# Optimization experiments

Measured on AMD Instinct MI355X. Metric: run time of the kernel, lower is better.

The kernel has to match this reference:

```python
import jax, jax.numpy as jnp
import numpy as np

NU, NBU, NI, D, L = 50000, 20000, 100000, 64, 2
C_TEMP = 0.25


def setup_inputs() -> dict:
    key = jax.random.key(0)
    ks = jax.random.split(key, 11)
    B, E_ui, E_ub, E_bi = 2048, 1_500_000, 1_000_000, 1_000_000
    return {
        "users": jax.random.randint(ks[0], (B,), 0, NU, dtype=jnp.int32),
        "bundles": jax.random.randint(ks[1], (B, 2), 0, NBU, dtype=jnp.int32),
        "ui_u": jax.random.randint(ks[2], (E_ui,), 0, NU, dtype=jnp.int32),
        "ui_i": jax.random.randint(ks[3], (E_ui,), 0, NI, dtype=jnp.int32),
        "ub_u": jax.random.randint(ks[4], (E_ub,), 0, NU, dtype=jnp.int32),
        "ub_b": jax.random.randint(ks[5], (E_ub,), 0, NBU, dtype=jnp.int32),
        "bi_b": jax.random.randint(ks[6], (E_bi,), 0, NBU, dtype=jnp.int32),
        "bi_i": jax.random.randint(ks[7], (E_bi,), 0, NI, dtype=jnp.int32),
        "users_feature": jax.random.normal(ks[8], (NU, D), jnp.float32) * 0.1,
        "bundles_feature": jax.random.normal(ks[9], (NBU, D), jnp.float32) * 0.1,
        "items_feature": jax.random.normal(ks[10], (NI, D), jnp.float32) * 0.1,
    }


def _sym_norm_vals(rows, cols, n):
    # laplace_transform: D_r^{-1/2} A D_c^{-1/2}; graph is symmetric so row/col degrees coincide
    deg = jax.ops.segment_sum(jnp.ones(rows.shape, jnp.float32), rows, num_segments=n)
    dinv = 1.0 / (jnp.sqrt(deg) + 1e-8)
    return dinv[rows] * dinv[cols]


def _spmm(rows, cols, vals, feat, n):
    return jax.ops.segment_sum(vals[:, None] * feat[cols], rows, num_segments=n)


def _one_propagate(rows, cols, n, A, Bf):
    vals = _sym_norm_vals(rows, cols, n)
    f = jnp.concatenate([A, Bf], axis=0)  # [n, D]
    acc = f
    for i in range(L):
        f = _spmm(rows, cols, vals, f, n) / (i + 2)
        nrm = jnp.maximum(jnp.linalg.norm(f, axis=1, keepdims=True), 1e-12)
        acc = acc + f / nrm  # sum of L2-normalized layer outputs + layer0
    return acc[: A.shape[0]], acc[A.shape[0]:]


def _bundle_agg(bi_b, bi_i, il_items):
    # row-normalized bundle-item aggregation: diag(1/bundle_size) @ BI
    deg = jax.ops.segment_sum(jnp.ones(bi_b.shape, jnp.float32), bi_b, num_segments=NBU)
    w = (1.0 / (deg + 1e-8))[bi_b]
    return jax.ops.segment_sum(w[:, None] * il_items[bi_i], bi_b, num_segments=NBU)


def _c_loss(pos, aug):
    pos = pos[:, 0, :]
    aug = aug[:, 0, :]
    pos = pos / jnp.maximum(jnp.linalg.norm(pos, axis=1, keepdims=True), 1e-12)
    aug = aug / jnp.maximum(jnp.linalg.norm(aug, axis=1, keepdims=True), 1e-12)
    pos_score = jnp.sum(pos * aug, axis=1) / C_TEMP
    ttl = jnp.matmul(pos, aug.T) / C_TEMP  # [B, B]
    return -jnp.mean(pos_score - jax.nn.logsumexp(ttl, axis=1))


def reference(users, bundles, ui_u, ui_i, ub_u, ub_b, bi_b, bi_i,
              users_feature, bundles_feature, items_feature):
    # item-level graph: [[0, UI], [UI^T, 0]], size NU+NI (symmetric directed edge list)
    il_rows = jnp.concatenate([ui_u, ui_i + NU])
    il_cols = jnp.concatenate([ui_i + NU, ui_u])
    IL_users, IL_items = _one_propagate(il_rows, il_cols, NU + NI, users_feature, items_feature)
    IL_bundles = _bundle_agg(bi_b, bi_i, IL_items)

    # bundle-level graph: [[0, UB], [UB^T, 0]], size NU+NBU
    bl_rows = jnp.concatenate([ub_u, ub_b + NU])
    bl_cols = jnp.concatenate([ub_b + NU, ub_u])
    BL_users, BL_bundles = _one_propagate(bl_rows, bl_cols, NU + NBU, users_feature, bundles_feature)

    nb = bundles.shape[1]
    IL_u = jnp.broadcast_to(IL_users[users][:, None, :], (users.shape[0], nb, D))
    BL_u = jnp.broadcast_to(BL_users[users][:, None, :], (users.shape[0], nb, D))
    IL_b = IL_bundles[bundles]  # [B, nb, D]
    BL_b = BL_bundles[bundles]

    pred = jnp.sum(IL_u * IL_b, axis=2) + jnp.sum(BL_u * BL_b, axis=2)  # [B, 2]
    bpr_loss = -jnp.mean(jax.nn.log_sigmoid(pred[:, 0:1] - pred[:, 1:2]))

    c_loss = 0.5 * (_c_loss(IL_u, BL_u) + _c_loss(IL_b, BL_b))
    return jnp.stack([bpr_loss, c_loss])


if __name__ == "__main__":
    out = reference(**setup_inputs())
    print(out)
```

## Files before the change

### kernel.cpp

```cpp
#include <hip/hip_runtime.h>
#include <hip/hip_bf16.h>
#include <math.h>

static constexpr int NUc  = 50000;
static constexpr int NBUc = 20000;
static constexpr int NIc  = 100000;
static constexpr int NILc = 150000;
static constexpr int NBLc = 70000;
static constexpr int GUB0   = 150016;
static constexpr int GBI0   = 220032;
static constexpr int BK_UB0 = 1172;
static constexpr int BK_BI0 = 1719;
static constexpr int NBK    = 1876;
static constexpr int GTOT   = NBK * 128;

__device__ __forceinline__ float wredsum(float v) {
  #pragma unroll
  for (int m = 32; m >= 1; m >>= 1) v += __shfl_xor(v, m, 64);
  return v;
}
__device__ __forceinline__ float bf2f(unsigned short h) {
  return __uint_as_float(((unsigned int)h) << 16);
}
__device__ __forceinline__ unsigned short f2bf(float f) {
  unsigned int u = __float_as_uint(f);
  return (unsigned short)((u + 0x7FFFu + ((u >> 16) & 1u)) >> 16);
}

__global__ void k_bcount_all(const int* __restrict__ ui_u, const int* __restrict__ ui_i,
                             const int* __restrict__ ub_u, const int* __restrict__ ub_b,
                             const int* __restrict__ bi_b,
                             int E_ui, int E_ub, int E_bi, int* __restrict__ bCnt) {
  __shared__ int hist[NBK];
  for (int i = threadIdx.x; i < NBK; i += 256) hist[i] = 0;
  __syncthreads();
  int b = blockIdx.x;
  if (b < 512) {
    int chunk = (E_ui + 511) / 512, c0 = b * chunk, c1 = min(E_ui, c0 + chunk);
    for (int e = c0 + (int)threadIdx.x; e < c1; e += 256) {
      atomicAdd(&hist[ui_u[e] >> 7], 1);
      atomicAdd(&hist[(ui_i[e] + NUc) >> 7], 1);
    }
  } else if (b < 768) {
    int lb = b - 512, chunk = (E_ub + 255) / 256, c0 = lb * chunk, c1 = min(E_ub, c0 + chunk);
    for (int e = c0 + (int)threadIdx.x; e < c1; e += 256) {
      atomicAdd(&hist[(GUB0 + ub_u[e]) >> 7], 1);
      atomicAdd(&hist[(GUB0 + NUc + ub_b[e]) >> 7], 1);
    }
  } else {
    int lb = b - 768, chunk = (E_bi + 255) / 256, c0 = lb * chunk, c1 = min(E_bi, c0 + chunk);
    for (int e = c0 + (int)threadIdx.x; e < c1; e += 256)
      atomicAdd(&hist[(GBI0 + bi_b[e]) >> 7], 1);
  }
  __syncthreads();
  for (int i = threadIdx.x; i < NBK; i += 256)
    if (hist[i]) atomicAdd(&bCnt[i], hist[i]);
}

__global__ void k_scan2048(const int* __restrict__ in, int n,
                           int* __restrict__ outBase, int* __restrict__ outCur) {
  __shared__ int sh[512];
  int t = threadIdx.x, i0 = 4 * t;
  int v0 = (i0 < n) ? in[i0] : 0;
  int v1 = (i0 + 1 < n) ? in[i0 + 1] : 0;
  int v2 = (i0 + 2 < n) ? in[i0 + 2] : 0;
  int v3 = (i0 + 3 < n) ? in[i0 + 3] : 0;
  int ts = v0 + v1 + v2 + v3;
  sh[t] = ts;
  __syncthreads();
  for (int o = 1; o < 512; o <<= 1) {
    int x = (t >= o) ? sh[t - o] : 0;
    __syncthreads();
    sh[t] += x;
    __syncthreads();
  }
  int ex = sh[t] - ts;
  if (i0 < n)     { outBase[i0] = ex;                    outCur[i0] = ex; }
  if (i0 + 1 < n) { outBase[i0 + 1] = ex + v0;           outCur[i0 + 1] = ex + v0; }
  if (i0 + 2 < n) { outBase[i0 + 2] = ex + v0 + v1;      outCur[i0 + 2] = ex + v0 + v1; }
  if (i0 + 3 < n) { outBase[i0 + 3] = ex + v0 + v1 + v2; outCur[i0 + 3] = ex + v0 + v1 + v2; }
  if (t == 511) outBase[n] = sh[511];
}

__global__ void k_bin_all(const int* __restrict__ ui_u, const int* __restrict__ ui_i,
                          const int* __restrict__ ub_u, const int* __restrict__ ub_b,
                          const int* __restrict__ bi_b, const int* __restrict__ bi_i,
                          int E_ui, int E_ub, int E_bi,
                          int* __restrict__ bCur, unsigned int* __restrict__ binned) {
  __shared__ int hist[NBK];
  __shared__ int base[NBK];
  for (int i = threadIdx.x; i < NBK; i += 256) hist[i] = 0;
  __syncthreads();
  int b = blockIdx.x;
  int c0, c1, seg;
  if (b < 512)      { seg = 0; int ch = (E_ui + 511) / 512; c0 = b * ch; c1 = min(E_ui, c0 + ch); }
  else if (b < 768) { seg = 1; int ch = (E_ub + 255) / 256; c0 = (b - 512) * ch; c1 = min(E_ub, c0 + ch); }
  else              { seg = 2; int ch = (E_bi + 255) / 256; c0 = (b - 768) * ch; c1 = min(E_bi, c0 + ch); }
  for (int e = c0 + (int)threadIdx.x; e < c1; e += 256) {
    if (seg == 0) {
      atomicAdd(&hist[ui_u[e] >> 7], 1);
      atomicAdd(&hist[(ui_i[e] + NUc) >> 7], 1);
    } else if (seg == 1) {
      atomicAdd(&hist[(GUB0 + ub_u[e]) >> 7], 1);
      atomicAdd(&hist[(GUB0 + NUc + ub_b[e]) >> 7], 1);
    } else {
      atomicAdd(&hist[(GBI0 + bi_b[e]) >> 7], 1);
    }
  }
  __syncthreads();
  for (int i = threadIdx.x; i < NBK; i += 256) {
    int h = hist[i];
    base[i] = h ? atomicAdd(&bCur[i], h) : 0;
    hist[i] = 0;
  }
  __syncthreads();
  for (int e = c0 + (int)threadIdx.x; e < c1; e += 256) {
    if (seg == 0) {
      int u = ui_u[e], x = ui_i[e] + NUc;
      int b1 = u >> 7;
      binned[base[b1] + atomicAdd(&hist[b1], 1)] = ((unsigned)(u & 127) << 18) | (unsigned)x;
      int b2 = x >> 7;
      binned[base[b2] + atomicAdd(&hist[b2], 1)] = ((unsigned)(x & 127) << 18) | (unsigned)u;
    } else if (seg == 1) {
      int ul = ub_u[e], bl = NUc + ub_b[e];
      int r1 = GUB0 + ul, r2 = GUB0 + bl;
      int b1 = r1 >> 7;
      binned[base[b1] + atomicAdd(&hist[b1], 1)] = ((unsigned)(r1 & 127) << 18) | (unsigned)bl;
      int b2 = r2 >> 7;
      binned[base[b2] + atomicAdd(&hist[b2], 1)] = ((unsigned)(r2 & 127) << 18) | (unsigned)ul;
    } else {
      int r = GBI0 + bi_b[e];
      int b1 = r >> 7;
      binned[base[b1] + atomicAdd(&hist[b1], 1)] = ((unsigned)(r & 127) << 18) | (unsigned)bi_i[e];
    }
  }
}

__global__ void k_rowhist_all(const unsigned int* __restrict__ binned, const int* __restrict__ bBase,
                              int* __restrict__ cnt) {
  __shared__ int hist[128];
  int bk = blockIdx.x, rowbase = bk << 7;
  int s = bBase[bk], e = bBase[bk + 1];
  if (threadIdx.x < 128) hist[threadIdx.x] = 0;
  __syncthreads();
  for (int i = s + (int)threadIdx.x; i < e; i += 256)
    atomicAdd(&hist[binned[i] >> 18], 1);
  __syncthreads();
  if (threadIdx.x < 128) cnt[rowbase + (int)threadIdx.x] = hist[threadIdx.x];
}

__global__ void k_scan_block_pad(const int* __restrict__ in, int n, int* __restrict__ out,
                                 int* __restrict__ bsum) {
  __shared__ int sh[256];
  int t = threadIdx.x;
  long base = (long)blockIdx.x * 1024 + (long)t * 4;
  int v0 = (base     < n) ? ((in[base]     + 15) & ~15) : 0;
  int v1 = (base + 1 < n) ? ((in[base + 1] + 15) & ~15) : 0;
  int v2 = (base + 2 < n) ? ((in[base + 2] + 15) & ~15) : 0;
  int v3 = (base + 3 < n) ? ((in[base + 3] + 15) & ~15) : 0;
  int tsum = v0 + v1 + v2 + v3;
  sh[t] = tsum;
  __syncthreads();
  for (int o = 1; o < 256; o <<= 1) {
    int x = (t >= o) ? sh[t - o] : 0;
    __syncthreads();
    sh[t] += x;
    __syncthreads();
  }
  int excl = sh[t] - tsum;
  if (t == 255) bsum[blockIdx.x] = sh[255];
  if (base     < n) out[base]     = excl;
  if (base + 1 < n) out[base + 1] = excl + v0;
  if (base + 2 < n) out[base + 2] = excl + v0 + v1;
  if (base + 3 < n) out[base + 3] = excl + v0 + v1 + v2;
}

__global__ void k_scan_bsum(int* __restrict__ bsum, int nb) {
  __shared__ int sh[256];
  int t = threadIdx.x;
  int v = (t < nb) ? bsum[t] : 0;
  sh[t] = v;
  __syncthreads();
  for (int o = 1; o < 256; o <<= 1) {
    int x = (t >= o) ? sh[t - o] : 0;
    __syncthreads();
    sh[t] += x;
    __syncthreads();
  }
  if (t < nb) bsum[t] = sh[t] - v;
}

__global__ void k_scan_add(int* __restrict__ out, int n, const int* __restrict__ bsum) {
  long i = (long)blockIdx.x * 256 + threadIdx.x;
  if (i < n) out[i] += bsum[i >> 10];
}

__global__ void k_csrfill_all(const unsigned int* __restrict__ binned, const int* __restrict__ bBase,
                              const int* __restrict__ rp, int* __restrict__ colv) {
  __shared__ int cur[128];
  int bk = blockIdx.x, rowbase = bk << 7;
  int xb, zpad;
  if (bk < BK_UB0)      { xb = 0;    zpad = NILc; }
  else if (bk < BK_BI0) { xb = GUB0; zpad = GUB0 + NBLc; }
  else                  { xb = 0;    zpad = NIc; }
  int s = bBase[bk], e = bBase[bk + 1];
  if (threadIdx.x < 128) cur[threadIdx.x] = rp[rowbase + (int)threadIdx.x];
  __syncthreads();
  for (int i = s + (int)threadIdx.x; i < e; i += 256) {
    unsigned int pk = binned[i];
    int pos = atomicAdd(&cur[pk >> 18], 1);
    colv[pos] = xb + (int)(pk & 0x3FFFFu);
  }
  __syncthreads();
  if (threadIdx.x < 128) {
    int r = rowbase + (int)threadIdx.x;
    int end = rp[r + 1];
    for (int k = cur[threadIdx.x]; k < end; k++) colv[k] = zpad;
  }
}

__global__ void k_prescale_all(const int* __restrict__ cnt, const float* __restrict__ userF,
                               const float* __restrict__ bundF, const float* __restrict__ itemF,
                               unsigned short* __restrict__ X) {
  long idx = (long)blockIdx.x * 256 + threadIdx.x;
  if (idx >= (long)GBI0 * 64) return;
  int g = (int)(idx >> 6), d = (int)(idx & 63);
  float v = 0.0f;
  if (g < NILc) v = (g < NUc) ? userF[(long)g * 64 + d] : itemF[(long)(g - NUc) * 64 + d];
  else if (g >= GUB0 && g < GUB0 + NBLc) {
    int l = g - GUB0;
    v = (l < NUc) ? userF[(long)l * 64 + d] : bundF[(long)(l - NUc) * 64 + d];
  }
  float dinv = 1.0f / (sqrtf((float)cnt[g]) + 1e-8f);
  X[idx] = f2bf(v * dinv);
}

__global__ void k_spmm_g(const int* __restrict__ rp, const int* __restrict__ cnt,
                         const int* __restrict__ col, const unsigned short* __restrict__ X,
                         unsigned short* __restrict__ outB, float* __restrict__ outInv,
                         float scale, int mulDinv, int n) {
  int row = blockIdx.x * 4 + (threadIdx.x >> 6);
  if (row >= n) return;
  int lane = threadIdx.x & 63, q = lane >> 4, p = lane & 15;
  int s = rp[row], e = rp[row + 1];
  const uint2* Xp = (const uint2*)X + p;
  float a0 = 0.f, a1 = 0.f, a2 = 0.f, a3 = 0.f;
  for (int eo = s + q; eo < e; eo += 16) {
    int c0 = col[eo], c1 = col[eo + 4], c2 = col[eo + 8], c3 = col[eo + 12];
    uint2 v0 = Xp[(size_t)c0 << 4];
    uint2 v1 = Xp[(size_t)c1 << 4];
    uint2 v2 = Xp[(size_t)c2 << 4];
    uint2 v3 = Xp[(size_t)c3 << 4];
    a0 += (__uint_as_float(v0.x << 16) + __uint_as_float(v1.x << 16)) +
          (__uint_as_float(v2.x << 16) + __uint_as_float(v3.x << 16));
    a1 += (__uint_as_float(v0.x & 0xFFFF0000u) + __uint_as_float(v1.x & 0xFFFF0000u)) +
          (__uint_as_float(v2.x & 0xFFFF0000u) + __uint_as_float(v3.x & 0xFFFF0000u));
    a2 += (__uint_as_float(v0.y << 16) + __uint_as_float(v1.y << 16)) +
          (__uint_as_float(v2.y << 16) + __uint_as_float(v3.y << 16));
    a3 += (__uint_as_float(v0.y & 0xFFFF0000u) + __uint_as_float(v1.y & 0xFFFF0000u)) +
          (__uint_as_float(v2.y & 0xFFFF0000u) + __uint_as_float(v3.y & 0xFFFF0000u));
  }
  a0 += __shfl_xor(a0, 32, 64); a1 += __shfl_xor(a1, 32, 64);
  a2 += __shfl_xor(a2, 32, 64); a3 += __shfl_xor(a3, 32, 64);
  a0 += __shfl_xor(a0, 16, 64); a1 += __shfl_xor(a1, 16, 64);
  a2 += __shfl_xor(a2, 16, 64); a3 += __shfl_xor(a3, 16, 64);
  float dinv = 1.0f / (sqrtf((float)cnt[row]) + 1e-8f);
  float f = dinv * scale;
  float r0 = a0 * f, r1 = a1 * f, r2 = a2 * f, r3 = a3 * f;
  float ss = r0 * r0 + r1 * r1 + r2 * r2 + r3 * r3;
  ss += __shfl_xor(ss, 8, 64); ss += __shfl_xor(ss, 4, 64);
  ss += __shfl_xor(ss, 2, 64); ss += __shfl_xor(ss, 1, 64);
  if (q == 0) {
    float mf = mulDinv ? dinv : 1.0f;
    uint2 m;
    m.x = (unsigned int)f2bf(r0 * mf) | ((unsigned int)f2bf(r1 * mf) << 16);
    m.y = (unsigned int)f2bf(r2 * mf) | ((unsigned int)f2bf(r3 * mf) << 16);
    *(uint2*)(outB + (size_t)row * 64 + p * 4) = m;
    if (p == 0) outInv[row] = 1.0f / fmaxf(sqrtf(ss), 1e-12f);
  }
}

__global__ void k_agg_g(const int* __restrict__ rp, const int* __restrict__ cnt,
                        const int* __restrict__ col, const unsigned short* __restrict__ MACC,
                        float* __restrict__ ILB, int n) {
  int rl = blockIdx.x * 4 + (threadIdx.x >> 6);
  if (rl >= n) return;
  int row = GBI0 + rl;
  int lane = threadIdx.x & 63, q = lane >> 4, p = lane & 15;
  int s = rp[row], e = rp[row + 1];
  const uint2* Xp = (const uint2*)MACC + p;
  float a0 = 0.f, a1 = 0.f, a2 = 0.f, a3 = 0.f;
  for (int eo = s + q; eo < e; eo += 16) {
    int c0 = col[eo], c1 = col[eo + 4], c2 = col[eo + 8], c3 = col[eo + 12];
    uint2 v0 = Xp[(size_t)c0 << 4];
    uint2 v1 = Xp[(size_t)c1 << 4];
    uint2 v2 = Xp[(size_t)c2 << 4];
    uint2 v3 = Xp[(size_t)c3 << 4];
    a0 += (__uint_as_float(v0.x << 16) + __uint_as_float(v1.x << 16)) +
          (__uint_as_float(v2.x << 16) + __uint_as_float(v3.x << 16));
    a1 += (__uint_as_float(v0.x & 0xFFFF0000u) + __uint_as_float(v1.x & 0xFFFF0000u)) +
          (__uint_as_float(v2.x & 0xFFFF0000u) + __uint_as_float(v3.x & 0xFFFF0000u));
    a2 += (__uint_as_float(v0.y << 16) + __uint_as_float(v1.y << 16)) +
          (__uint_as_float(v2.y << 16) + __uint_as_float(v3.y << 16));
    a3 += (__uint_as_float(v0.y & 0xFFFF0000u) + __uint_as_float(v1.y & 0xFFFF0000u)) +
          (__uint_as_float(v2.y & 0xFFFF0000u) + __uint_as_float(v3.y & 0xFFFF0000u));
  }
  a0 += __shfl_xor(a0, 32, 64); a1 += __shfl_xor(a1, 32, 64);
  a2 += __shfl_xor(a2, 32, 64); a3 += __shfl_xor(a3, 32, 64);
  a0 += __shfl_xor(a0, 16, 64); a1 += __shfl_xor(a1, 16, 64);
  a2 += __shfl_xor(a2, 16, 64); a3 += __shfl_xor(a3, 16, 64);
  if (q == 0) {
    float w = 1.0f / ((float)cnt[row] + 1e-8f);
    *(float4*)(ILB + (size_t)rl * 64 + p * 4) = make_float4(a0 * w, a1 * w, a2 * w, a3 * w);
  }
}

__global__ void k_acc_items(const float* __restrict__ itemF, const int* __restrict__ cnt,
                            const unsigned short* __restrict__ M1, const unsigned short* __restrict__ F2b,
                            const float* __restrict__ INV1, const float* __restrict__ INV2,
                            unsigned short* __restrict__ MACC) {
  long idx = (long)blockIdx.x * 256 + threadIdx.x;
  if (idx >= (long)NIc * 64) return;
  int rl = (int)(idx >> 6);
  int g = NUc + rl;
  long gi = (long)g * 64 + (idx & 63);
  float rs = sqrtf((float)cnt[g]) + 1e-8f;
  float res = itemF[idx] + bf2f(M1[gi]) * rs * INV1[g] + bf2f(F2b[gi]) * INV2[g];
  MACC[idx] = f2bf(res);
}

__global__ void k_batch(const int* __restrict__ users, const int* __restrict__ bundles,
                        const float* __restrict__ userF, const float* __restrict__ bundF,
                        const int* __restrict__ cnt,
                        const unsigned short* __restrict__ M1, const unsigned short* __restrict__ F2b,
                        const float* __restrict__ INV1, const float* __restrict__ INV2,
                        const float* __restrict__ ILB, int B,
                        float* __restrict__ ILu, float* __restrict__ BLu,
                        float* __restrict__ ILb2, float* __restrict__ BLb2,
                        float* __restrict__ PN1, float* __restrict__ AN1,
                        float* __restrict__ PN2, float* __restrict__ AN2) {
  int w = blockIdx.x * 4 + (threadIdx.x >> 6);
  int lane = threadIdx.x & 63;
  if (w >= 6 * B) return;
  float val;
  float* rawDst; float* nrmDst = nullptr; int nrmRow = 0;
  if (w < 2 * B) {
    bool il = w < B;
    int j = il ? w : w - B;
    int u = users[j];
    int g = il ? u : GUB0 + u;
    long gi = (long)g * 64 + lane;
    float rs = sqrtf((float)cnt[g]) + 1e-8f;
    val = userF[(long)u * 64 + lane] + bf2f(M1[gi]) * rs * INV1[g] + bf2f(F2b[gi]) * INV2[g];
    rawDst = (il ? ILu : BLu) + (long)j * 64;
    nrmDst = il ? PN1 : AN1; nrmRow = j;
  } else if (w < 4 * B) {
    int j = w - 2 * B;
    int b = bundles[j];
    val = ILB[(long)b * 64 + lane];
    rawDst = ILb2 + (long)j * 64;
    if ((j & 1) == 0) { nrmDst = PN2; nrmRow = j >> 1; }
  } else {
    int j = w - 4 * B;
    int b = bundles[j];
    int g = GUB0 + NUc + b;
    long gi = (long)g * 64 + lane;
    float rs = sqrtf((float)cnt[g]) + 1e-8f;
    val = bundF[(long)b * 64 + lane] + bf2f(M1[gi]) * rs * INV1[g] + bf2f(F2b[gi]) * INV2[g];
    rawDst = BLb2 + (long)j * 64;
    if ((j & 1) == 0) { nrmDst = AN2; nrmRow = j >> 1; }
  }
  rawDst[lane] = val;
  float ss = wredsum(val * val);
  if (nrmDst) nrmDst[(long)nrmRow * 64 + lane] = val * (1.0f / fmaxf(sqrtf(ss), 1e-12f));
}

__global__ void k_bpr(const float* __restrict__ ILu, const float* __restrict__ ILb2,
                      const float* __restrict__ BLu, const float* __restrict__ BLb2,
                      int B, float* __restrict__ out) {
  int row = blockIdx.x * 4 + (threadIdx.x >> 6);
  int lane = threadIdx.x & 63;
  if (row >= B) return;
  float t = ILu[(long)row * 64 + lane] *
              (ILb2[(long)(2 * row) * 64 + lane] - ILb2[(long)(2 * row + 1) * 64 + lane]) +
            BLu[(long)row * 64 + lane] *
              (BLb2[(long)(2 * row) * 64 + lane] - BLb2[(long)(2 * row + 1) * 64 + lane]);
  float x = wredsum(t);
  if (lane == 0) {
    float ls = -(fmaxf(-x, 0.0f) + log1pf(expf(-fabsf(x))));
    unsafeAtomicAdd(&out[0], -ls / (float)B);
  }
}

__global__ void k_gemm_nt2(const float* __restrict__ P1, const float* __restrict__ A1,
                           const float* __restrict__ P2, const float* __restrict__ A2,
                           float* __restrict__ S1o, float* __restrict__ S2o,
                           int N, float scale) {
  __shared__ float Ps[64][129];
  __shared__ float As[64][129];
  const float* P = blockIdx.z ? P2 : P1;
  const float* A = blockIdx.z ? A2 : A1;
  float* S = blockIdx.z ? S2o : S1o;
  int bi0 = blockIdx.y * 128, bj0 = blockIdx.x * 128;
  int t = threadIdx.x;
  #pragma unroll
  for (int sct = 0; sct < 8; sct++) {
    int idx4 = t + sct * 256;
    int r = idx4 >> 4, k = (idx4 & 15) << 2;
    int pr = min(bi0 + r, N - 1);
    int ar = min(bj0 + r, N - 1);
    float4 v = *(const float4*)(P + (long)pr * 64 + k);
    Ps[k][r] = v.x; Ps[k + 1][r] = v.y; Ps[k + 2][r] = v.z; Ps[k + 3][r] = v.w;
    float4 w = *(const float4*)(A + (long)ar * 64 + k);
    As[k][r] = w.x; As[k + 1][r] = w.y; As[k + 2][r] = w.z; As[k + 3][r] = w.w;
  }
  __syncthreads();
  int tx = t & 15, ty = t >> 4;
  float acc[8][8];
  #pragma unroll
  for (int i = 0; i < 8; i++)
    #pragma unroll
    for (int j = 0; j < 8; j++) acc[i][j] = 0.0f;
  #pragma unroll 4
  for (int k = 0; k < 64; k++) {
    float a[8], b[8];
    #pragma unroll
    for (int i = 0; i < 8; i++) a[i] = Ps[k][ty * 8 + i];
    #pragma unroll
    for (int j = 0; j < 8; j++) b[j] = As[k][tx + 16 * j];
    #pragma unroll
    for (int i = 0; i < 8; i++)
      #pragma unroll
      for (int j = 0; j < 8; j++) acc[i][j] = fmaf(a[i], b[j], acc[i][j]);
  }
  #pragma unroll
  for (int i = 0; i < 8; i++) {
    int row = bi0 + ty * 8 + i;
    if (row >= N) continue;
    #pragma unroll
    for (int j = 0; j < 8; j++) {
      int cc = bj0 + tx + 16 * j;
      if (cc < N) S[(long)row * N + cc] = acc[i][j] * scale;
    }
  }
}

__global__ void k_lse2(const float* __restrict__ S1, const float* __restrict__ S2,
                       int B, float coeff, float* __restrict__ out) {
  constexpr float L2E = 1.44269504f;
  int row = blockIdx.x * 4 + (threadIdx.x >> 6);
  int lane = threadIdx.x & 63;
  const float* Sr; int dg;
  if (row < B) { Sr = S1 + (long)row * B; dg = row; }
  else         { Sr = S2 + (long)(row - B) * B; dg = row - B; }
  float m = -1e30f, s = 0.0f;
  for (int w = 0; w < (B >> 8); w++) {
    float4 v = *(const float4*)(Sr + ((w << 6) + lane) * 4);
    float mx = fmaxf(fmaxf(v.x, v.y), fmaxf(v.z, v.w));
    if (mx > m) { s *= exp2f((m - mx) * L2E); m = mx; }
    s += exp2f((v.x - m) * L2E) + exp2f((v.y - m) * L2E) +
         exp2f((v.z - m) * L2E) + exp2f((v.w - m) * L2E);
  }
  #pragma unroll
  for (int o = 32; o >= 1; o >>= 1) {
    float m2 = __shfl_xor(m, o, 64), s2 = __shfl_xor(s, o, 64);
    float M = fmaxf(m, m2);
    s = s * exp2f((m - M) * L2E) + s2 * exp2f((m2 - M) * L2E);
    m = M;
  }
  if (lane == 0) {
    float lse = m + log2f(s) * 0.69314718f;
    unsafeAtomicAdd(&out[1], -(Sr[dg] - lse) * coeff);
  }
}

extern "C" void kernel_launch(void* const* d_in, const int* in_sizes, int n_in,
                              void* d_out, int out_size, void* d_ws, size_t ws_size,
                              hipStream_t stream) {
  const int* users   = (const int*)d_in[0];
  const int* bundles = (const int*)d_in[1];
  const int* ui_u    = (const int*)d_in[2];
  const int* ui_i    = (const int*)d_in[3];
  const int* ub_u    = (const int*)d_in[4];
  const int* ub_b    = (const int*)d_in[5];
  const int* bi_b    = (const int*)d_in[6];
  const int* bi_i    = (const int*)d_in[7];
  const float* userF = (const float*)d_in[8];
  const float* bundF = (const float*)d_in[9];
  const float* itemF = (const float*)d_in[10];
  float* out = (float*)d_out;

  const int B    = in_sizes[0];
  const int E_ui = in_sizes[2];
  const int E_ub = in_sizes[4];
  const int E_bi = in_sizes[6];
  const long E_all = 2L * E_ui + 2L * E_ub + E_bi;

  float* ws = (float*)d_ws;
  size_t off = 0;
  auto alloc = [&](size_t nfloat) -> float* {
    float* p = ws + off;
    off += (nfloat + 63) & ~(size_t)63;
    return p;
  };
  unsigned short* X  = (unsigned short*)alloc((size_t)GBI0 * 32);
  unsigned short* M1 = (unsigned short*)alloc((size_t)GBI0 * 32);
  unsigned int* binned = (unsigned int*)alloc((size_t)E_all);
  int* colv  = (int*)alloc((size_t)E_all + 15 * (size_t)GTOT + 128);
  int* rp    = (int*)alloc(GTOT + 1);
  int* cnt   = (int*)alloc(GTOT + 1);
  float* INV1 = alloc(GTOT);
  float* INV2 = alloc(GTOT);
  float* ILB  = alloc((size_t)NBUc * 64);
  float* ILu  = alloc((size_t)B * 64);
  float* BLu  = alloc((size_t)B * 64);
  float* ILb2 = alloc((size_t)B * 128);
  float* BLb2 = alloc((size_t)B * 128);
  float* PN1  = alloc((size_t)B * 64);
  float* AN1  = alloc((size_t)B * 64);
  float* PN2  = alloc((size_t)B * 64);
  float* AN2  = alloc((size_t)B * 64);
  int* bCnt  = (int*)alloc(2049);
  int* bBase = (int*)alloc(2049);
  int* bCur  = (int*)alloc(2049);
  int* bsum  = (int*)alloc(256);
  (void)ws_size; (void)n_in; (void)out_size;

  unsigned short* F2b  = X;
  unsigned short* MACC = (unsigned short*)binned;
  float* S1 = (float*)X;
  float* S2 = (float*)M1;

  hipMemsetAsync(bCnt, 0, sizeof(int) * NBK, stream);
  k_bcount_all<<<1024, 256, 0, stream>>>(ui_u, ui_i, ub_u, ub_b, bi_b, E_ui, E_ub, E_bi, bCnt);
  k_scan2048<<<1, 512, 0, stream>>>(bCnt, NBK, bBase, bCur);
  k_bin_all<<<1024, 256, 0, stream>>>(ui_u, ui_i, ub_u, ub_b, bi_b, bi_i,
                                      E_ui, E_ub, E_bi, bCur, binned);
  hipMemsetAsync(cnt, 0, sizeof(int) * (GTOT + 1), stream);
  k_rowhist_all<<<NBK, 256, 0, stream>>>(binned, bBase, cnt);
  {
    int scan_n = GTOT + 1;
    int nb1 = (scan_n + 1023) / 1024;
    k_scan_block_pad<<<nb1, 256, 0, stream>>>(cnt, scan_n, rp, bsum);
    k_scan_bsum<<<1, 256, 0, stream>>>(bsum, nb1);
    k_scan_add<<<(scan_n + 255) / 256, 256, 0, stream>>>(rp, scan_n, bsum);
  }
  k_csrfill_all<<<NBK, 256, 0, stream>>>(binned, bBase, rp, colv);

  k_prescale_all<<<(int)(((long)GBI0 * 64 + 255) / 256), 256, 0, stream>>>(cnt, userF, bundF,
                                                                           itemF, X);
  k_spmm_g<<<(GBI0 + 3) / 4, 256, 0, stream>>>(rp, cnt, colv, X, M1, INV1, 0.5f, 1, GBI0);
  k_spmm_g<<<(GBI0 + 3) / 4, 256, 0, stream>>>(rp, cnt, colv, M1, F2b, INV2, 1.0f / 3.0f, 0, GBI0);
  hipMemsetAsync(MACC + (size_t)NIc * 64, 0, 128, stream);
  k_acc_items<<<(int)(((long)NIc * 64 + 255) / 256), 256, 0, stream>>>(
      itemF, cnt, M1, F2b, INV1, INV2, MACC);
  k_agg_g<<<(NBUc + 3) / 4, 256, 0, stream>>>(rp, cnt, colv, MACC, ILB, NBUc);
  k_batch<<<(6 * B + 3) / 4, 256, 0, stream>>>(users, bundles, userF, bundF, cnt, M1, F2b,
                                               INV1, INV2, ILB, B,
                                               ILu, BLu, ILb2, BLb2, PN1, AN1, PN2, AN2);

  hipMemsetAsync(out, 0, 2 * sizeof(float), stream);
  k_bpr<<<(B + 3) / 4, 256, 0, stream>>>(ILu, ILb2, BLu, BLb2, B, out);
  dim3 gg((B + 127) / 128, (B + 127) / 128, 2);
  k_gemm_nt2<<<gg, 256, 0, stream>>>(PN1, AN1, PN2, AN2, S1, S2, B, 4.0f);
  k_lse2<<<(2 * B + 3) / 4, 256, 0, stream>>>(S1, S2, B, 0.5f / (float)B, out);
}
```

Before: 531.7 us.

## Fuse contrastive logsumexp into GEMM epilogue and drop bf16 high-half masking

The contrastive-loss GEMM no longer writes the full BxB score matrices. Each block now computes a per-row partial max and sum-exp over its 128-column tile, plus the diagonal entry, and a small final kernel merges the 16 partials per row. This removes the write and re-read of two 2048x2048 fp32 matrices. Separately, the SpMM and aggregation inner loops reinterpret packed bf16 pairs as floats without masking the low half, saving ALU ops. That leaves tiny low-mantissa noise in the odd channels, which slightly changes numerics.

After: 526.0 us. No clear change (-1.1%).

```diff
diff --git a/kernel.cpp b/kernel.cpp
--- a/kernel.cpp
+++ b/kernel.cpp
@@ -253,12 +253,12 @@
     uint2 v3 = Xp[(size_t)c3 << 4];
     a0 += (__uint_as_float(v0.x << 16) + __uint_as_float(v1.x << 16)) +
           (__uint_as_float(v2.x << 16) + __uint_as_float(v3.x << 16));
-    a1 += (__uint_as_float(v0.x & 0xFFFF0000u) + __uint_as_float(v1.x & 0xFFFF0000u)) +
-          (__uint_as_float(v2.x & 0xFFFF0000u) + __uint_as_float(v3.x & 0xFFFF0000u));
+    a1 += (__uint_as_float(v0.x) + __uint_as_float(v1.x)) +
+          (__uint_as_float(v2.x) + __uint_as_float(v3.x));
     a2 += (__uint_as_float(v0.y << 16) + __uint_as_float(v1.y << 16)) +
           (__uint_as_float(v2.y << 16) + __uint_as_float(v3.y << 16));
-    a3 += (__uint_as_float(v0.y & 0xFFFF0000u) + __uint_as_float(v1.y & 0xFFFF0000u)) +
-          (__uint_as_float(v2.y & 0xFFFF0000u) + __uint_as_float(v3.y & 0xFFFF0000u));
+    a3 += (__uint_as_float(v0.y) + __uint_as_float(v1.y)) +
+          (__uint_as_float(v2.y) + __uint_as_float(v3.y));
   }
   a0 += __shfl_xor(a0, 32, 64); a1 += __shfl_xor(a1, 32, 64);
   a2 += __shfl_xor(a2, 32, 64); a3 += __shfl_xor(a3, 32, 64);
@@ -298,12 +298,12 @@
     uint2 v3 = Xp[(size_t)c3 << 4];
     a0 += (__uint_as_float(v0.x << 16) + __uint_as_float(v1.x << 16)) +
           (__uint_as_float(v2.x << 16) + __uint_as_float(v3.x << 16));
-    a1 += (__uint_as_float(v0.x & 0xFFFF0000u) + __uint_as_float(v1.x & 0xFFFF0000u)) +
-          (__uint_as_float(v2.x & 0xFFFF0000u) + __uint_as_float(v3.x & 0xFFFF0000u));
+    a1 += (__uint_as_float(v0.x) + __uint_as_float(v1.x)) +
+          (__uint_as_float(v2.x) + __uint_as_float(v3.x));
     a2 += (__uint_as_float(v0.y << 16) + __uint_as_float(v1.y << 16)) +
           (__uint_as_float(v2.y << 16) + __uint_as_float(v3.y << 16));
-    a3 += (__uint_as_float(v0.y & 0xFFFF0000u) + __uint_as_float(v1.y & 0xFFFF0000u)) +
-          (__uint_as_float(v2.y & 0xFFFF0000u) + __uint_as_float(v3.y & 0xFFFF0000u));
+    a3 += (__uint_as_float(v0.y) + __uint_as_float(v1.y)) +
+          (__uint_as_float(v2.y) + __uint_as_float(v3.y));
   }
   a0 += __shfl_xor(a0, 32, 64); a1 += __shfl_xor(a1, 32, 64);
   a2 += __shfl_xor(a2, 32, 64); a3 += __shfl_xor(a3, 32, 64);
@@ -392,15 +392,15 @@
   }
 }
 
-__global__ void k_gemm_nt2(const float* __restrict__ P1, const float* __restrict__ A1,
+__global__ void k_gemm_lse(const float* __restrict__ P1, const float* __restrict__ A1,
                            const float* __restrict__ P2, const float* __restrict__ A2,
-                           float* __restrict__ S1o, float* __restrict__ S2o,
-                           int N, float scale) {
-  __shared__ float Ps[64][129];
-  __shared__ float As[64][129];
+                           float* __restrict__ Pm, float* __restrict__ Ps,
+                           float* __restrict__ Diag, int N, float scale) {
+  __shared__ float PsS[64][129];
+  __shared__ float AsS[64][129];
+  constexpr float L2E = 1.44269504f;
   const float* P = blockIdx.z ? P2 : P1;
   const float* A = blockIdx.z ? A2 : A1;
-  float* S = blockIdx.z ? S2o : S1o;
   int bi0 = blockIdx.y * 128, bj0 = blockIdx.x * 128;
   int t = threadIdx.x;
   #pragma unroll
@@ -410,9 +410,9 @@
     int pr = min(bi0 + r, N - 1);
     int ar = min(bj0 + r, N - 1);
     float4 v = *(const float4*)(P + (long)pr * 64 + k);
-    Ps[k][r] = v.x; Ps[k + 1][r] = v.y; Ps[k + 2][r] = v.z; Ps[k + 3][r] = v.w;
+    PsS[k][r] = v.x; PsS[k + 1][r] = v.y; PsS[k + 2][r] = v.z; PsS[k + 3][r] = v.w;
     float4 w = *(const float4*)(A + (long)ar * 64 + k);
-    As[k][r] = w.x; As[k + 1][r] = w.y; As[k + 2][r] = w.z; As[k + 3][r] = w.w;
+    AsS[k][r] = w.x; AsS[k + 1][r] = w.y; AsS[k + 2][r] = w.z; AsS[k + 3][r] = w.w;
   }
   __syncthreads();
   int tx = t & 15, ty = t >> 4;
@@ -425,44 +425,55 @@
   for (int k = 0; k < 64; k++) {
     float a[8], b[8];
     #pragma unroll
-    for (int i = 0; i < 8; i++) a[i] = Ps[k][ty * 8 + i];
-    #pragma unroll
-    for (int j = 0; j < 8; j++) b[j] = As[k][tx + 16 * j];
+    for (int i = 0; i < 8; i++) a[i] = PsS[k][ty * 8 + i];
+    #pragma unroll
+    for (int j = 0; j < 8; j++) b[j] = AsS[k][tx + 16 * j];
     #pragma unroll
     for (int i = 0; i < 8; i++)
       #pragma unroll
       for (int j = 0; j < 8; j++) acc[i][j] = fmaf(a[i], b[j], acc[i][j]);
   }
+  bool diagBlk = (blockIdx.x == blockIdx.y);
   #pragma unroll
   for (int i = 0; i < 8; i++) {
-    int row = bi0 + ty * 8 + i;
-    if (row >= N) continue;
-    #pragma unroll
-    for (int j = 0; j < 8; j++) {
-      int cc = bj0 + tx + 16 * j;
-      if (cc < N) S[(long)row * N + cc] = acc[i][j] * scale;
+    int lrow = ty * 8 + i;
+    float xs[8], tm = -1e30f;
+    #pragma unroll
+    for (int j = 0; j < 8; j++) { xs[j] = acc[i][j] * scale; tm = fmaxf(tm, xs[j]); }
+    float tsum = 0.f;
+    #pragma unroll
+    for (int j = 0; j < 8; j++) tsum += exp2f((xs[j] - tm) * L2E);
+    #pragma unroll
+    for (int o = 1; o <= 8; o <<= 1) {
+      float m2 = __shfl_xor(tm, o, 64), s2 = __shfl_xor(tsum, o, 64);
+      float M = fmaxf(tm, m2);
+      tsum = tsum * exp2f((tm - M) * L2E) + s2 * exp2f((m2 - M) * L2E);
+      tm = M;
     }
-  }
-}
-
-__global__ void k_lse2(const float* __restrict__ S1, const float* __restrict__ S2,
-                       int B, float coeff, float* __restrict__ out) {
+    if (tx == 0) {
+      size_t o = ((size_t)blockIdx.z * N + bi0 + lrow) * 16 + blockIdx.x;
+      Pm[o] = tm; Ps[o] = tsum;
+    }
+    if (diagBlk && tx == (lrow & 15))
+      Diag[(size_t)blockIdx.z * N + bi0 + lrow] = xs[lrow >> 4];
+  }
+}
+
+__global__ void k_lse_final(const float* __restrict__ Pm, const float* __restrict__ Ps,
+                            const float* __restrict__ Diag, int N, float coeff,
+                            float* __restrict__ out) {
   constexpr float L2E = 1.44269504f;
-  int row = blockIdx.x * 4 + (threadIdx.x >> 6);
+  int idx = blockIdx.x * 4 + (threadIdx.x >> 6);
+  if (idx >= 2 * N) return;
+  int z = idx >= N ? 1 : 0, r = idx - z * N;
   int lane = threadIdx.x & 63;
-  const float* Sr; int dg;
-  if (row < B) { Sr = S1 + (long)row * B; dg = row; }
-  else         { Sr = S2 + (long)(row - B) * B; dg = row - B; }
-  float m = -1e30f, s = 0.0f;
-  for (int w = 0; w < (B >> 8); w++) {
-    float4 v = *(const float4*)(Sr + ((w << 6) + lane) * 4);
-    float mx = fmaxf(fmaxf(v.x, v.y), fmaxf(v.z, v.w));
-    if (mx > m) { s *= exp2f((m - mx) * L2E); m = mx; }
-    s += exp2f((v.x - m) * L2E) + exp2f((v.y - m) * L2E) +
-         exp2f((v.z - m) * L2E) + exp2f((v.w - m) * L2E);
+  float m = -1e30f, s = 0.f;
+  if (lane < 16) {
+    size_t o = ((size_t)z * N + r) * 16 + lane;
+    m = Pm[o]; s = Ps[o];
   }
   #pragma unroll
-  for (int o = 32; o >= 1; o >>= 1) {
+  for (int o = 8; o >= 1; o >>= 1) {
     float m2 = __shfl_xor(m, o, 64), s2 = __shfl_xor(s, o, 64);
     float M = fmaxf(m, m2);
     s = s * exp2f((m - M) * L2E) + s2 * exp2f((m2 - M) * L2E);
@@ -470,7 +481,7 @@
   }
   if (lane == 0) {
     float lse = m + log2f(s) * 0.69314718f;
-    unsafeAtomicAdd(&out[1], -(Sr[dg] - lse) * coeff);
+    unsafeAtomicAdd(&out[1], -(Diag[(size_t)z * N + r] - lse) * coeff);
   }
 }
 
@@ -520,6 +531,9 @@
   float* AN1  = alloc((size_t)B * 64);
   float* PN2  = alloc((size_t)B * 64);
   float* AN2  = alloc((size_t)B * 64);
+  float* Pm   = alloc((size_t)2 * B * 16);
+  float* Ps   = alloc((size_t)2 * B * 16);
+  float* Diag = alloc((size_t)2 * B);
   int* bCnt  = (int*)alloc(2049);
   int* bBase = (int*)alloc(2049);
   int* bCur  = (int*)alloc(2049);
@@ -528,8 +542,6 @@
 
   unsigned short* F2b  = X;
   unsigned short* MACC = (unsigned short*)binned;
-  float* S1 = (float*)X;
-  float* S2 = (float*)M1;
 
   hipMemsetAsync(bCnt, 0, sizeof(int) * NBK, stream);
   k_bcount_all<<<1024, 256, 0, stream>>>(ui_u, ui_i, ub_u, ub_b, bi_b, E_ui, E_ub, E_bi, bCnt);
@@ -562,6 +574,6 @@
   hipMemsetAsync(out, 0, 2 * sizeof(float), stream);
   k_bpr<<<(B + 3) / 4, 256, 0, stream>>>(ILu, ILb2, BLu, BLb2, B, out);
   dim3 gg((B + 127) / 128, (B + 127) / 128, 2);
-  k_gemm_nt2<<<gg, 256, 0, stream>>>(PN1, AN1, PN2, AN2, S1, S2, B, 4.0f);
-  k_lse2<<<(2 * B + 3) / 4, 256, 0, stream>>>(S1, S2, B, 0.5f / (float)B, out);
-}
+  k_gemm_lse<<<gg, 256, 0, stream>>>(PN1, AN1, PN2, AN2, Pm, Ps, Diag, B, 4.0f);
+  k_lse_final<<<(2 * B + 3) / 4, 256, 0, stream>>>(Pm, Ps, Diag, B, 0.5f / (float)B, out);
+}
```
